# Optimization experiments

Hardware: AMD Instinct MI355X
Metric: run time of the kernel (lower is better)

The kernel has to match this reference:

```python
import jax, jax.numpy as jnp
from jax import lax
import numpy as np

D_MODEL = 512
D_STATE = 16
D_CONV = 4
EXPAND = 2
D_INNER = EXPAND * D_MODEL  # 1024
DT_RANK = (D_MODEL + 15) // 16  # 32
FF_DIM = 1024
N_LAYERS = 2
B, L = 2, 2048


def setup_inputs() -> dict:
    key = jax.random.key(0)
    ks = jax.random.split(key, 16)
    s = 0.02
    x = jax.random.normal(ks[0], (B, L, D_MODEL), jnp.float32)
    in_proj_w = jax.random.normal(ks[1], (N_LAYERS, 2 * D_INNER, D_MODEL), jnp.float32) * s
    conv_w = jax.random.normal(ks[2], (N_LAYERS, D_INNER, D_CONV), jnp.float32) * 0.3
    conv_b = jax.random.normal(ks[3], (N_LAYERS, D_INNER), jnp.float32) * s
    x_proj_w = jax.random.normal(ks[4], (N_LAYERS, DT_RANK + 2 * D_STATE, D_INNER), jnp.float32) * s
    dt_proj_w = jax.random.normal(ks[5], (N_LAYERS, D_INNER, DT_RANK), jnp.float32) * s
    dt_proj_b = jax.random.normal(ks[6], (N_LAYERS, D_INNER), jnp.float32) * 0.5 - 4.0
    A_log = jnp.log(jnp.broadcast_to(jnp.arange(1, D_STATE + 1, dtype=jnp.float32), (N_LAYERS, D_INNER, D_STATE)))
    Dp = jnp.ones((N_LAYERS, D_INNER), jnp.float32)
    out_proj_w = jax.random.normal(ks[7], (N_LAYERS, D_MODEL, D_INNER), jnp.float32) * s
    mlp_w1 = jax.random.normal(ks[8], (FF_DIM, D_MODEL), jnp.float32) * s
    mlp_b1 = jnp.zeros((FF_DIM,), jnp.float32)
    mlp_w2 = jax.random.normal(ks[9], (D_MODEL, FF_DIM), jnp.float32) * s
    mlp_b2 = jnp.zeros((D_MODEL,), jnp.float32)
    return dict(x=x, in_proj_w=in_proj_w, conv_w=conv_w, conv_b=conv_b,
                x_proj_w=x_proj_w, dt_proj_w=dt_proj_w, dt_proj_b=dt_proj_b,
                A_log=A_log, Dp=Dp, out_proj_w=out_proj_w,
                mlp_w1=mlp_w1, mlp_b1=mlp_b1, mlp_w2=mlp_w2, mlp_b2=mlp_b2)


def _mamba_layer(x, ipw, cw, cb, xpw, dpw, dpb, Al, Dv, opw):
    # x: [B, L, d_model]
    b, l, _ = x.shape
    xz = jnp.einsum('bld,ed->ble', x, ipw)           # [B, L, 2*d_inner]
    xin, z = jnp.split(xz, 2, axis=-1)
    # causal depthwise conv1d (pad left d_conv-1)
    xc = jnp.transpose(xin, (0, 2, 1))               # [B, d_inner, L]
    xc = lax.conv_general_dilated(xc, cw[:, None, :], (1,), [(D_CONV - 1, 0)],
                                  feature_group_count=D_INNER)
    xin = jax.nn.silu(jnp.transpose(xc + cb[:, None], (0, 2, 1)))  # [B, L, d_inner]
    dbl = jnp.einsum('bld,ed->ble', xin, xpw)        # [B, L, dt_rank + 2*d_state]
    dt, Bm, Cm = jnp.split(dbl, [DT_RANK, DT_RANK + D_STATE], axis=-1)
    dt = jax.nn.softplus(jnp.einsum('blr,dr->bld', dt, dpw) + dpb)  # [B, L, d_inner]
    A = -jnp.exp(Al)                                  # [d_inner, d_state]
    dA = jnp.exp(dt[..., None] * A)                   # [B, L, d_inner, d_state]
    dBu = dt[..., None] * Bm[:, :, None, :] * xin[..., None]

    def step(h, inp):
        dA_t, dBu_t = inp
        h = dA_t * h + dBu_t
        return h, h

    h0 = jnp.zeros((b, D_INNER, D_STATE), x.dtype)
    _, hs = lax.scan(step, h0, (jnp.moveaxis(dA, 1, 0), jnp.moveaxis(dBu, 1, 0)))
    hs = jnp.moveaxis(hs, 0, 1)                       # [B, L, d_inner, d_state]
    y = jnp.einsum('blds,bls->bld', hs, Cm) + xin * Dv
    y = y * jax.nn.silu(z)
    return jnp.einsum('ble,de->bld', y, opw)


def reference(x, in_proj_w, conv_w, conv_b, x_proj_w, dt_proj_w, dt_proj_b,
              A_log, Dp, out_proj_w, mlp_w1, mlp_b1, mlp_w2, mlp_b2):
    residual = x
    for i in range(N_LAYERS):
        x = _mamba_layer(x, in_proj_w[i], conv_w[i], conv_b[i], x_proj_w[i],
                         dt_proj_w[i], dt_proj_b[i], A_log[i], Dp[i], out_proj_w[i])
    h = x + residual
    h = jax.nn.relu(jnp.einsum('bld,fd->blf', h, mlp_w1) + mlp_b1)  # dropout is identity in eval
    return jnp.einsum('blf,df->bld', h, mlp_w2) + mlp_b2
```

## Files before the change

kernel.cpp:

```cpp
#include <hip/hip_runtime.h>
#include <hip/hip_bf16.h>

#define BB 2
#define LL 2048
#define DMODEL 512
#define DSTATE 16
#define DINNER 1024
#define DTRANK 32
#define FFDIM 1024
#define MTOT (BB*LL)
#define SCL 64
#define NCC 32

typedef unsigned short u16;
typedef __attribute__((ext_vector_type(8))) short bf16x8;
typedef __attribute__((ext_vector_type(4))) float f32x4;

__device__ __forceinline__ float b2f(u16 u){
  unsigned v = ((unsigned)u) << 16; float f; __builtin_memcpy(&f, &v, 4); return f;
}
__device__ __forceinline__ u16 f2b(float f){
  unsigned u; __builtin_memcpy(&u, &f, 4);
  unsigned r = (u + 0x7FFFu + ((u >> 16) & 1u)) >> 16;
  return (u16)r;
}
__device__ __forceinline__ float siluf(float x){ return x / (1.f + __expf(-x)); }
__device__ __forceinline__ float softplusf(float v){
  return fmaxf(v, 0.f) + __logf(1.f + __expf(-fabsf(v)));
}

__device__ __forceinline__ float ldin(const void* p, size_t i, int bf){
  if (bf) return b2f(((const u16*)p)[i]);
  return ((const float*)p)[i];
}
__device__ __forceinline__ void stout(void* p, size_t i, int bf, float v){
  if (bf) ((u16*)p)[i] = f2b(v);
  else    ((float*)p)[i] = v;
}

__device__ __forceinline__ int getbf(const void* dp){
  return (*(const unsigned*)dp == 0x3F803F80u) ? 1 : 0;
}

template<int CVT>
__device__ __forceinline__ bf16x8 ld8(const void* P, size_t gi, int bf){
  if (!CVT || bf) return *(const bf16x8*)((const u16*)P + gi);
  float4 f0 = *(const float4*)((const float*)P + gi);
  float4 f1 = *(const float4*)((const float*)P + gi + 4);
  union { u16 u[8]; bf16x8 v; } t;
  t.u[0]=f2b(f0.x); t.u[1]=f2b(f0.y); t.u[2]=f2b(f0.z); t.u[3]=f2b(f0.w);
  t.u[4]=f2b(f1.x); t.u[5]=f2b(f1.y); t.u[6]=f2b(f1.z); t.u[7]=f2b(f1.w);
  return t.v;
}

#define CVT_IPW (2*2*DINNER*DMODEL)
#define CVT_XPW (2*64*DINNER)
#define CVT_DPW (2*DINNER*DTRANK)
#define CVT_OPW (2*DMODEL*DINNER)
#define CVT_W1  (FFDIM*DMODEL)
#define CVT_W2  (DMODEL*FFDIM)
#define CVT_CW  (2*DINNER*4)
#define CVT_CB  (2*DINNER)
#define CVT_TOT (CVT_IPW+CVT_XPW+CVT_DPW+CVT_OPW+CVT_W1+CVT_W2+CVT_CW+CVT_CB)
__global__ __launch_bounds__(256) void cvt_all_k(
    const void* __restrict__ ipw, const void* __restrict__ xpw,
    const void* __restrict__ dpw, const void* __restrict__ opw,
    const void* __restrict__ w1, const void* __restrict__ w2,
    const void* __restrict__ cw, const void* __restrict__ cb,
    u16* __restrict__ dst, const void* __restrict__ dprobe)
{
  const int bf = getbf(dprobe);
  size_t i4 = ((size_t)blockIdx.x * 256 + threadIdx.x) * 4;
  if (i4 >= CVT_TOT) return;
  const void* src; size_t off = i4;
  if      (off < CVT_IPW)                     { src = ipw; }
  else if ((off -= CVT_IPW) < CVT_XPW)        { src = xpw; }
  else if ((off -= CVT_XPW) < CVT_DPW)        { src = dpw; }
  else if ((off -= CVT_DPW) < CVT_OPW)        { src = opw; }
  else if ((off -= CVT_OPW) < CVT_W1)         { src = w1; }
  else if ((off -= CVT_W1)  < CVT_W2)         { src = w2; }
  else if ((off -= CVT_W2)  < CVT_CW)         { src = cw; }
  else     { off -= CVT_CW;                     src = cb; }
  ushort4 o;
  if (bf) {
    o = *(const ushort4*)((const u16*)src + off);
  } else {
    float4 f = *(const float4*)((const float*)src + off);
    o.x = f2b(f.x); o.y = f2b(f.y); o.z = f2b(f.z); o.w = f2b(f.w);
  }
  *(ushort4*)(dst + i4) = o;
}

template<int ACT, int CVA, int CVW, int CIN, int BM, int BN, int KB, int RESID>
__global__ __launch_bounds__(256) void gemm_mfma(
    const void* __restrict__ A, size_t aoff, int lda,
    const void* __restrict__ W, size_t woff,
    const void* __restrict__ bias, size_t boff,
    void* __restrict__ C, size_t coff, int ldc, int K,
    const void* __restrict__ xres, size_t xroff,
    const void* __restrict__ dprobe)
{
  const int bf = getbf(dprobe);
  constexpr int C8  = KB / 8;
  constexpr int TR  = 256 / C8;
  constexpr int ALD = BM / TR;
  constexpr int WLD = BN / TR;
  __shared__ __align__(16) u16 As[2][BM * KB];
  __shared__ __align__(16) u16 Ws[2][BN * KB];
  const int tid = threadIdx.x;
  const int row0 = blockIdx.y * BM, col0 = blockIdx.x * BN;
  const int wave = tid >> 6, lane = tid & 63;
  const int l15 = lane & 15, quad = lane >> 4;
  constexpr int WMT = (BM == 64) ? 1 : ((BN == 128) ? 4 : 2);
  const int mbase = (BM == 64) ? (wave * 16)
                  : ((BN == 128) ? (wave & 1) * 64 : wave * 32);
  const int nbase = (BM == 128 && BN == 128) ? (wave >> 1) * 64 : 0;

  const int rT = tid / C8, csw = tid % C8;
  const int scg = (KB == 32) ? (csw ^ ((rT >> 1) & 3)) : (csw ^ (rT & 7));
  const int lws = tid * 8;
  const size_t ab0 = aoff + (size_t)(row0 + rT) * lda + scg * 8;
  const size_t wb0 = woff + (size_t)(col0 + rT) * K   + scg * 8;

  f32x4 acc[WMT][4];
#pragma unroll
  for (int i = 0; i < WMT; i++)
#pragma unroll
    for (int j = 0; j < 4; j++) acc[i][j] = (f32x4){0.f,0.f,0.f,0.f};

  const int NT = K / KB;

  auto fchunk = [&](int r_, int g){
    return (KB == 32) ? (g ^ ((r_ >> 1) & 3)) : (g ^ (r_ & 7));
  };
  auto compute = [&](int cur_){
#pragma unroll
    for (int ks = 0; ks < KB / 32; ks++) {
      bf16x8 af_[WMT], bf_[4];
#pragma unroll
      for (int mt = 0; mt < WMT; mt++) {
        int r_ = mbase + mt * 16 + l15;
        af_[mt] = *(const bf16x8*)&As[cur_][r_ * KB + fchunk(r_, ks * 4 + quad) * 8];
      }
#pragma unroll
      for (int nt = 0; nt < 4; nt++) {
        int r_ = nbase + nt * 16 + l15;
        bf_[nt] = *(const bf16x8*)&Ws[cur_][r_ * KB + fchunk(r_, ks * 4 + quad) * 8];
      }
#pragma unroll
      for (int mt = 0; mt < WMT; mt++)
#pragma unroll
        for (int nt = 0; nt < 4; nt++)
          acc[mt][nt] = __builtin_amdgcn_mfma_f32_16x16x32_bf16(af_[mt], bf_[nt], acc[mt][nt], 0, 0, 0);
    }
  };

  bf16x8 ra0[ALD], rw0[WLD], ra1[ALD], rw1[WLD];

#define GLOAD(RA, RW, T) do { const int k1_ = (T) * KB;                        \
  _Pragma("unroll") for (int i = 0; i < ALD; i++)                              \
    RA[i] = ld8<CVA>(A, ab0 + k1_ + (size_t)i * TR * lda, bf);                 \
  _Pragma("unroll") for (int i = 0; i < WLD; i++)                              \
    RW[i] = ld8<CVW>(W, wb0 + k1_ + (size_t)i * TR * K, bf); } while (0)

#define GSTEP(RA, RW, T) do {                                                  \
  const int cur_ = (T) & 1;                                                    \
  _Pragma("unroll") for (int i = 0; i < ALD; i++)                              \
    *(bf16x8*)&As[cur_][lws + i * 2048] = RA[i];                               \
  _Pragma("unroll") for (int i = 0; i < WLD; i++)                              \
    *(bf16x8*)&Ws[cur_][lws + i * 2048] = RW[i];                               \
  if ((T) + 2 < NT) GLOAD(RA, RW, (T) + 2);                                    \
  __syncthreads();                                                             \
  compute(cur_);                                                               \
} while (0)

  GLOAD(ra0, rw0, 0);
  if (NT > 1) GLOAD(ra1, rw1, 1);
  int t = 0;
  for (; t + 1 < NT; t += 2) { GSTEP(ra0, rw0, t); GSTEP(ra1, rw1, t + 1); }
  if (t < NT) GSTEP(ra0, rw0, t);
#undef GLOAD
#undef GSTEP

#pragma unroll
  for (int nt = 0; nt < 4; nt++) {
    int c = col0 + nbase + nt * 16 + l15;
    float bv = bias ? ldin(bias, boff + c, bf) : 0.f;
#pragma unroll
    for (int mt = 0; mt < WMT; mt++) {
      int rb = row0 + mbase + mt * 16 + quad * 4;
#pragma unroll
      for (int r = 0; r < 4; r++) {
        float v = acc[mt][nt][r] + bv;
        if (ACT == 1) v = softplusf(v);
        if (ACT == 2) v = fmaxf(v, 0.f);
        size_t ci = (size_t)(rb + r) * ldc + c;
        if (RESID) v += ldin(xres, xroff + ci, bf);
        if (CIN) stout(C, coff + ci, bf, v);
        else     ((u16*)C)[coff + ci] = f2b(v);
      }
    }
  }
}

template<int FST>
__global__ __launch_bounds__(256) void conv_k(
    const u16* __restrict__ xz, const void* __restrict__ cw, size_t cwo,
    const void* __restrict__ cb, size_t cbo, u16* __restrict__ xc,
    const void* __restrict__ dprobe)
{
  if (FST) {
    const u16* cw16 = (const u16*)cw;
    const u16* cb16 = (const u16*)cb;
    int idx8 = (blockIdx.x * 256 + threadIdx.x) * 8;
    int d8 = idx8 & 1023;
    int row = idx8 >> 10;
    int lb = row & (LL - 1);
    bf16x8 cwv0 = *(const bf16x8*)&cw16[cwo + d8*4];
    bf16x8 cwv1 = *(const bf16x8*)&cw16[cwo + d8*4 + 8];
    bf16x8 cwv2 = *(const bf16x8*)&cw16[cwo + d8*4 + 16];
    bf16x8 cwv3 = *(const bf16x8*)&cw16[cwo + d8*4 + 24];
    bf16x8 cbv  = *(const bf16x8*)&cb16[cbo + d8];
    bf16x8 xv0 = (bf16x8){0,0,0,0,0,0,0,0}, xv1 = xv0, xv2 = xv0, xv3 = xv0;
    if (lb >= 3) xv0 = *(const bf16x8*)&xz[(size_t)(row - 3) * 2048 + d8];
    if (lb >= 2) xv1 = *(const bf16x8*)&xz[(size_t)(row - 2) * 2048 + d8];
    if (lb >= 1) xv2 = *(const bf16x8*)&xz[(size_t)(row - 1) * 2048 + d8];
    xv3 = *(const bf16x8*)&xz[(size_t)row * 2048 + d8];
    bf16x8 ov;
#pragma unroll
    for (int i = 0; i < 8; i++) {
      float acc = b2f((u16)cbv[i]);
      int c0 = i * 4;
      float w0 = b2f((u16)((c0 < 8) ? cwv0[c0 & 7] : (c0 < 16) ? cwv1[c0 & 7] : (c0 < 24) ? cwv2[c0 & 7] : cwv3[c0 & 7]));
      float w1_ = b2f((u16)(((c0+1) < 8) ? cwv0[(c0+1) & 7] : ((c0+1) < 16) ? cwv1[(c0+1) & 7] : ((c0+1) < 24) ? cwv2[(c0+1) & 7] : cwv3[(c0+1) & 7]));
      float w2_ = b2f((u16)(((c0+2) < 8) ? cwv0[(c0+2) & 7] : ((c0+2) < 16) ? cwv1[(c0+2) & 7] : ((c0+2) < 24) ? cwv2[(c0+2) & 7] : cwv3[(c0+2) & 7]));
      float w3_ = b2f((u16)(((c0+3) < 8) ? cwv0[(c0+3) & 7] : ((c0+3) < 16) ? cwv1[(c0+3) & 7] : ((c0+3) < 24) ? cwv2[(c0+3) & 7] : cwv3[(c0+3) & 7]));
      acc += w0 * b2f((u16)xv0[i]);
      acc += w1_ * b2f((u16)xv1[i]);
      acc += w2_ * b2f((u16)xv2[i]);
      acc += w3_ * b2f((u16)xv3[i]);
      ov[i] = (short)f2b(siluf(acc));
    }
    *(bf16x8*)&xc[idx8] = ov;
  } else {
    const int bf = getbf(dprobe);
    int idx = blockIdx.x * 256 + threadIdx.x;
    int d = idx & 1023;
    int row = idx >> 10;
    int lb = row & (LL - 1);
    float acc = ldin(cb, cbo + d, bf);
#pragma unroll
    for (int k = 0; k < 4; k++) {
      int lk = lb - 3 + k;
      if (lk >= 0) acc += ldin(cw, cwo + d*4 + k, bf) * b2f(xz[(size_t)(row - 3 + k) * 2048 + d]);
    }
    xc[idx] = f2b(siluf(acc));
  }
}

template<int CVW>
__global__ __launch_bounds__(256) void scan_A_k(
    const u16* __restrict__ xc,
    const u16* __restrict__ dbl,
    const void* __restrict__ dpwp, size_t dpwo,
    const void* __restrict__ dpbp, size_t dpbo,
    const void* __restrict__ Alog, size_t alo,
    float* __restrict__ Pc, float* __restrict__ Sc,
    const void* __restrict__ dprobe)
{
  const int bf = getbf(dprobe);
  int bid = blockIdx.x;
  int b = bid >> 9;
  int c = (bid >> 4) & (NCC - 1);
  int g = bid & 15;
  int t = threadIdx.x;
  int dl = t >> 2, sq = t & 3;
  int d0 = g * 64, d = d0 + dl;
  int rowb = b * LL + c * SCL;

  __shared__ __align__(16) u16 dts[64 * 64];
  __shared__ __align__(16) u16 us[64 * 64];
  __shared__ __align__(16) float Bs[64 * 20];
  u16* dbls = dts;
  u16* dpws = dts + 64 * 32;

  {
    int r = t >> 2, c8 = (t & 3) * 8;
    *(bf16x8*)&dbls[r * 32 + c8] =
        *(const bf16x8*)&dbl[(size_t)(rowb + r) * 64 + c8];
    *(bf16x8*)&dpws[r * 32 + c8] =
        ld8<CVW>(dpwp, dpwo + (size_t)(d0 + r) * DTRANK + c8, bf);
  }
#pragma unroll
  for (int p = 0; p < 2; p++) {
    int seg = p * 256 + t;
    int r = seg >> 3, c8 = (seg & 7) * 8;
    bf16x8 uv = *(const bf16x8*)&xc[(size_t)(rowb + r) * 1024 + d0 + c8];
    int coff = r >> 3, roff = r & 7;
#pragma unroll
    for (int i = 0; i < 8; i++) {
      int dd = c8 + i;
      us[dd * 64 + ((coff ^ (dd & 7)) << 3) + roff] = (u16)uv[i];
    }
  }
  if (t < 128) {
    int l = t >> 1, grp = t & 1;
    bf16x8 v = *(const bf16x8*)&dbl[(size_t)(rowb + l) * 64 + 32 + grp * 8];
    f32x4 f0 = {b2f((u16)v[0]), b2f((u16)v[1]), b2f((u16)v[2]), b2f((u16)v[3])};
    f32x4 f1 = {b2f((u16)v[4]), b2f((u16)v[5]), b2f((u16)v[6]), b2f((u16)v[7])};
    *(f32x4*)&Bs[l * 20 + grp * 8]     = f0;
    *(f32x4*)&Bs[l * 20 + grp * 8 + 4] = f1;
  }
  float Av[4];
#pragma unroll
  for (int j = 0; j < 4; j++)
    Av[j] = -__expf(ldin(Alog, alo + (size_t)d * DSTATE + sq * 4 + j, bf));
  __syncthreads();

  {
    int wv = t >> 6, lane = t & 63;
    int fl = lane & 15, qd = lane >> 4;
    bf16x8 afr  = *(const bf16x8*)&dbls[(wv * 16 + fl) * 32 + qd * 8];
    bf16x8 bfr0 = *(const bf16x8*)&dpws[(fl)      * 32 + qd * 8];
    bf16x8 bfr1 = *(const bf16x8*)&dpws[(16 + fl) * 32 + qd * 8];
    bf16x8 bfr2 = *(const bf16x8*)&dpws[(32 + fl) * 32 + qd * 8];
    bf16x8 bfr3 = *(const bf16x8*)&dpws[(48 + fl) * 32 + qd * 8];
    __syncthreads();
    f32x4 zz = {0.f, 0.f, 0.f, 0.f};
    f32x4 a0 = __builtin_amdgcn_mfma_f32_16x16x32_bf16(afr, bfr0, zz, 0, 0, 0);
    f32x4 a1 = __builtin_amdgcn_mfma_f32_16x16x32_bf16(afr, bfr1, zz, 0, 0, 0);
    f32x4 a2 = __builtin_amdgcn_mfma_f32_16x16x32_bf16(afr, bfr2, zz, 0, 0, 0);
    f32x4 a3 = __builtin_amdgcn_mfma_f32_16x16x32_bf16(afr, bfr3, zz, 0, 0, 0);
    int lc = wv * 2 + (qd >> 1);
    int off = (qd & 1) * 4;
#define DTWR(AN, NT) do {                                                      \
    int dd_ = (NT) * 16 + fl;                                                  \
    float bvv_ = ldin(dpbp, dpbo + d0 + dd_, bf);                              \
    ushort4 pk_;                                                               \
    pk_.x = f2b(softplusf(AN[0] + bvv_));                                      \
    pk_.y = f2b(softplusf(AN[1] + bvv_));                                      \
    pk_.z = f2b(softplusf(AN[2] + bvv_));                                      \
    pk_.w = f2b(softplusf(AN[3] + bvv_));                                      \
    *(ushort4*)&dts[dd_ * 64 + ((lc ^ (dd_ & 7)) << 3) + off] = pk_; } while (0)
    DTWR(a0, 0); DTWR(a1, 1); DTWR(a2, 2); DTWR(a3, 3);
#undef DTWR
  }
  __syncthreads();

  float h[4] = {0.f,0.f,0.f,0.f}, P[4] = {1.f,1.f,1.f,1.f};
  for (int cc = 0; cc < 8; cc++) {
    int base = dl * 64 + ((cc ^ (dl & 7)) << 3);
    bf16x8 dt8 = *(const bf16x8*)&dts[base];
    bf16x8 u8  = *(const bf16x8*)&us[base];
#pragma unroll
    for (int i = 0; i < 8; i++) {
      int l = cc * 8 + i;
      float dtv = b2f((u16)dt8[i]);
      float uv  = b2f((u16)u8[i]);
      float dtu = dtv * uv;
      f32x4 B4 = *(const f32x4*)&Bs[l * 20 + sq * 4];
#pragma unroll
      for (int j = 0; j < 4; j++) {
        float dA = __expf(dtv * Av[j]);
        h[j] = dA * h[j] + dtu * B4[j];
        P[j] *= dA;
      }
    }
  }
  size_t o = (((size_t)b * DINNER + d) * NCC + c) * DSTATE + sq * 4;
  *(f32x4*)&Pc[o] = (f32x4){P[0], P[1], P[2], P[3]};
  *(f32x4*)&Sc[o] = (f32x4){h[0], h[1], h[2], h[3]};
}

__global__ __launch_bounds__(256) void scan_B_k(
    float* __restrict__ Pc, const float* __restrict__ Sc)
{
  int idx = blockIdx.x * 256 + threadIdx.x;
  int bd = idx >> 4, s = idx & 15;
  float h = 0.f;
  for (int c = 0; c < NCC; c++) {
    size_t o = ((size_t)bd * NCC + c) * DSTATE + s;
    float P = Pc[o], S = Sc[o];
    Pc[o] = h;
    h = P * h + S;
  }
}

template<int CVW>
__global__ __launch_bounds__(256) void scan_C_k(
    u16* __restrict__ dtp, int sdt, const u16* __restrict__ xz,
    const u16* __restrict__ xc,
    const u16* __restrict__ dbl,
    const void* __restrict__ dpwp, size_t dpwo,
    const void* __restrict__ dpbp, size_t dpbo,
    const void* __restrict__ Alog, size_t alo,
    const void* __restrict__ Dpt, size_t dpo, const float* __restrict__ Hinit,
    const void* __restrict__ dprobe)
{
  const int bf = getbf(dprobe);
  int bid = blockIdx.x;
  int b = bid >> 9;
  int c = (bid >> 4) & (NCC - 1);
  int g = bid & 15;
  int t = threadIdx.x;
  int dl = t >> 2, sq = t & 3;
  int d0 = g * 64, d = d0 + dl;
  int rowb = b * LL + c * SCL;

  __shared__ __align__(16) u16 dts[64 * 64];
  __shared__ __align__(16) u16 us[64 * 64];
  __shared__ __align__(16) u16 outs[64 * 64];
  __shared__ __align__(16) float BCs[64 * 36];
  u16* dbls = dts;
  u16* dpws = dts + 64 * 32;

  {
    int r = t >> 2, c8 = (t & 3) * 8;
    *(bf16x8*)&dbls[r * 32 + c8] =
        *(const bf16x8*)&dbl[(size_t)(rowb + r) * 64 + c8];
    *(bf16x8*)&dpws[r * 32 + c8] =
        ld8<CVW>(dpwp, dpwo + (size_t)(d0 + r) * DTRANK + c8, bf);
  }
#pragma unroll
  for (int p = 0; p < 2; p++) {
    int seg = p * 256 + t;
    int r = seg >> 3, c8 = (seg & 7) * 8;
    bf16x8 uv = *(const bf16x8*)&xc[(size_t)(rowb + r) * 1024 + d0 + c8];
    int coff = r >> 3, roff = r & 7;
#pragma unroll
    for (int i = 0; i < 8; i++) {
      int dd = c8 + i;
      us[dd * 64 + ((coff ^ (dd & 7)) << 3) + roff] = (u16)uv[i];
    }
  }
  {
    int l = t >> 2, grp = t & 3;
    bf16x8 v = *(const bf16x8*)&dbl[(size_t)(rowb + l) * 64 + 32 + grp * 8];
    f32x4 f0 = {b2f((u16)v[0]), b2f((u16)v[1]), b2f((u16)v[2]), b2f((u16)v[3])};
    f32x4 f1 = {b2f((u16)v[4]), b2f((u16)v[5]), b2f((u16)v[6]), b2f((u16)v[7])};
    *(f32x4*)&BCs[l * 36 + grp * 8]     = f0;
    *(f32x4*)&BCs[l * 36 + grp * 8 + 4] = f1;
  }
  float Av[4];
#pragma unroll
  for (int j = 0; j < 4; j++)
    Av[j] = -__expf(ldin(Alog, alo + (size_t)d * DSTATE + sq * 4 + j, bf));
  float Dv = ldin(Dpt, dpo + d, bf);
  float h[4];
  size_t o = (((size_t)b * DINNER + d) * NCC + c) * DSTATE + sq * 4;
  f32x4 h4 = *(const f32x4*)&Hinit[o];
  h[0] = h4[0]; h[1] = h4[1]; h[2] = h4[2]; h[3] = h4[3];
  __syncthreads();

  {
    int wv = t >> 6, lane = t & 63;
    int fl = lane & 15, qd = lane >> 4;
    bf16x8 afr  = *(const bf16x8*)&dbls[(wv * 16 + fl) * 32 + qd * 8];
    bf16x8 bfr0 = *(const bf16x8*)&dpws[(fl)      * 32 + qd * 8];
    bf16x8 bfr1 = *(const bf16x8*)&dpws[(16 + fl) * 32 + qd * 8];
    bf16x8 bfr2 = *(const bf16x8*)&dpws[(32 + fl) * 32 + qd * 8];
    bf16x8 bfr3 = *(const bf16x8*)&dpws[(48 + fl) * 32 + qd * 8];
    __syncthreads();
    f32x4 zz = {0.f, 0.f, 0.f, 0.f};
    f32x4 a0 = __builtin_amdgcn_mfma_f32_16x16x32_bf16(afr, bfr0, zz, 0, 0, 0);
    f32x4 a1 = __builtin_amdgcn_mfma_f32_16x16x32_bf16(afr, bfr1, zz, 0, 0, 0);
    f32x4 a2 = __builtin_amdgcn_mfma_f32_16x16x32_bf16(afr, bfr2, zz, 0, 0, 0);
    f32x4 a3 = __builtin_amdgcn_mfma_f32_16x16x32_bf16(afr, bfr3, zz, 0, 0, 0);
    int lc = wv * 2 + (qd >> 1);
    int off = (qd & 1) * 4;
#define DTWR(AN, NT) do {                                                      \
    int dd_ = (NT) * 16 + fl;                                                  \
    float bvv_ = ldin(dpbp, dpbo + d0 + dd_, bf);                              \
    ushort4 pk_;                                                               \
    pk_.x = f2b(softplusf(AN[0] + bvv_));                                      \
    pk_.y = f2b(softplusf(AN[1] + bvv_));                                      \
    pk_.z = f2b(softplusf(AN[2] + bvv_));                                      \
    pk_.w = f2b(softplusf(AN[3] + bvv_));                                      \
    *(ushort4*)&dts[dd_ * 64 + ((lc ^ (dd_ & 7)) << 3) + off] = pk_; } while (0)
    DTWR(a0, 0); DTWR(a1, 1); DTWR(a2, 2); DTWR(a3, 3);
#undef DTWR
  }
  __syncthreads();

  for (int cc = 0; cc < 8; cc++) {
    int base = dl * 64 + ((cc ^ (dl & 7)) << 3);
    bf16x8 dt8 = *(const bf16x8*)&dts[base];
    bf16x8 u8  = *(const bf16x8*)&us[base];
#pragma unroll
    for (int i = 0; i < 8; i++) {
      int l = cc * 8 + i;
      float dtv = b2f((u16)dt8[i]);
      float uv  = b2f((u16)u8[i]);
      float dtu = dtv * uv;
      f32x4 B4 = *(const f32x4*)&BCs[l * 36 + sq * 4];
      f32x4 C4 = *(const f32x4*)&BCs[l * 36 + 16 + sq * 4];
      float y = 0.f;
#pragma unroll
      for (int j = 0; j < 4; j++) {
        float dA = __expf(dtv * Av[j]);
        h[j] = dA * h[j] + dtu * B4[j];
        y += h[j] * C4[j];
      }
      y += __shfl_xor(y, 1);
      y += __shfl_xor(y, 2);
      if (sq == 0) outs[l * 64 + dl] = f2b(y + uv * Dv);
    }
  }
  __syncthreads();
#pragma unroll
  for (int p = 0; p < 2; p++) {
    int seg = p * 256 + t;
    int r = seg >> 3, c8 = (seg & 7) * 8;
    bf16x8 yv = *(const bf16x8*)&outs[r * 64 + c8];
    bf16x8 zv = *(const bf16x8*)&xz[(size_t)(rowb + r) * 2048 + 1024 + d0 + c8];
    bf16x8 ov;
#pragma unroll
    for (int i = 0; i < 8; i++) {
      float z = b2f((u16)zv[i]);
      ov[i] = (short)f2b(b2f((u16)yv[i]) * siluf(z));
    }
    *(bf16x8*)&dtp[(size_t)(rowb + r) * sdt + d0 + c8] = ov;
  }
}

extern "C" void kernel_launch(void* const* d_in, const int* in_sizes, int n_in,
                              void* d_out, int out_size, void* d_ws, size_t ws_size,
                              hipStream_t stream) {
  const void* x_in = d_in[0];
  const void* ipw  = d_in[1];
  const void* cw   = d_in[2];
  const void* cb   = d_in[3];
  const void* xpw  = d_in[4];
  const void* dpw  = d_in[5];
  const void* dpb  = d_in[6];
  const void* Alog = d_in[7];
  const void* Dpt  = d_in[8];
  const void* opw  = d_in[9];
  const void* w1   = d_in[10];
  const void* b1   = d_in[11];
  const void* w2   = d_in[12];
  const void* b2   = d_in[13];

  const bool full = ws_size >= (size_t)64 * 1024 * 1024;
  const bool bfh = (in_sizes[1] == (int)(CVT_IPW * 2));

  if (full) {
    float* Pc = (float*)((char*)d_ws + 64);
    float* Sc = Pc + (size_t)BB*DINNER*NCC*DSTATE;
    u16* p = (u16*)(Sc + (size_t)BB*DINNER*NCC*DSTATE);
    u16* cvt0  = p;
    u16* ipw16 = p;  p += (size_t)CVT_IPW;
    u16* xpw16 = p;  p += (size_t)CVT_XPW;
    u16* dpw16 = p;  p += (size_t)CVT_DPW;
    u16* opw16 = p;  p += (size_t)CVT_OPW;
    u16* w116  = p;  p += (size_t)CVT_W1;
    u16* w216  = p;  p += (size_t)CVT_W2;
    u16* cw16  = p;  p += (size_t)CVT_CW;
    u16* cb16  = p;  p += (size_t)CVT_CB;
    u16* xz    = p;  p += (size_t)MTOT*2*DINNER;
    u16* xc    = p;  p += (size_t)MTOT*DINNER;
    u16* dty   = p;  p += (size_t)MTOT*DINNER;
    u16* dbl   = p;
    u16* bx = xc;
    u16* resid = xz;
    u16* hid = xz + (size_t)4*1024*1024;

    const u16* Wipw = bfh ? (const u16*)ipw : ipw16;
    const u16* Wxpw = bfh ? (const u16*)xpw : xpw16;
    const u16* Wdpw = bfh ? (const u16*)dpw : dpw16;
    const u16* Wopw = bfh ? (const u16*)opw : opw16;
    const u16* Ww1  = bfh ? (const u16*)w1  : w116;
    const u16* Ww2  = bfh ? (const u16*)w2  : w216;
    const u16* Wcw  = bfh ? (const u16*)cw  : cw16;
    const u16* Wcb  = bfh ? (const u16*)cb  : cb16;
    if (!bfh)
      cvt_all_k<<<(CVT_TOT/4 + 255)/256, 256, 0, stream>>>(
          ipw, xpw, dpw, opw, w1, w2, cw, cb, cvt0, Dpt);

    for (int layer = 0; layer < 2; layer++) {
      size_t ipw_o = (size_t)layer*2*DINNER*DMODEL;
      size_t cw_o  = (size_t)layer*DINNER*4,  cb_o = (size_t)layer*DINNER;
      size_t xpw_o = (size_t)layer*64*DINNER, dpw_o = (size_t)layer*DINNER*DTRANK;
      size_t dpb_o = (size_t)layer*DINNER,    al_o = (size_t)layer*DINNER*DSTATE;
      size_t dp_o  = (size_t)layer*DINNER,    opw_o = (size_t)layer*DMODEL*DINNER;
      if (layer == 0)
        gemm_mfma<0,1,0,0,128,64,32,0><<<dim3(32, 32), 256, 0, stream>>>(
            x_in, 0, DMODEL, Wipw, ipw_o, nullptr, 0, xz, 0, 2048, DMODEL,
            nullptr, 0, Dpt);
      else
        gemm_mfma<0,0,0,0,128,64,32,0><<<dim3(32, 32), 256, 0, stream>>>(
            bx, 0, DMODEL, Wipw, ipw_o, nullptr, 0, xz, 0, 2048, DMODEL,
            nullptr, 0, Dpt);
      conv_k<1><<<MTOT*DINNER/2048, 256, 0, stream>>>(
          xz, Wcw, cw_o, Wcb, cb_o, xc, Dpt);
      gemm_mfma<0,0,0,0,64,64,32,0><<<dim3(1, 64), 256, 0, stream>>>(
          xc, 0, DINNER, Wxpw, xpw_o, nullptr, 0, dbl, 0, 64, DINNER,
          nullptr, 0, Dpt);
      scan_A_k<0><<<BB*NCC*16, 256, 0, stream>>>(
          xc, dbl, Wdpw, dpw_o, dpb, dpb_o, Alog, al_o, Pc, Sc, Dpt);
      scan_B_k<<<BB*64, 256, 0, stream>>>(Pc, Sc);
      scan_C_k<0><<<BB*NCC*16, 256, 0, stream>>>(
          dty, 1024, xz, xc, dbl, Wdpw, dpw_o, dpb, dpb_o, Alog, al_o,
          Dpt, dp_o, Pc, Dpt);
      if (layer == 0)
        gemm_mfma<0,0,0,0,64,64,32,0><<<dim3(8, 64), 256, 0, stream>>>(
            dty, 0, 1024, Wopw, opw_o, nullptr, 0, bx, 0, DMODEL, DINNER,
            nullptr, 0, Dpt);
      else
        gemm_mfma<0,0,0,0,64,64,32,1><<<dim3(8, 64), 256, 0, stream>>>(
            dty, 0, 1024, Wopw, opw_o, nullptr, 0, resid, 0, DMODEL, DINNER,
            x_in, 0, Dpt);
    }
    gemm_mfma<2,0,0,0,64,64,32,0><<<dim3(16, 64), 256, 0, stream>>>(
        resid, 0, DMODEL, Ww1, 0, b1, 0, hid, 0, FFDIM, DMODEL,
        nullptr, 0, Dpt);
    gemm_mfma<0,0,0,1,64,64,32,0><<<dim3(8, 64), 256, 0, stream>>>(
        hid, 0, FFDIM, Ww2, 0, b2, 0, d_out, 0, DMODEL, FFDIM,
        nullptr, 0, Dpt);
  } else {
    float* Pc = (float*)((char*)d_ws + 64);
    float* Sc = Pc + (size_t)DINNER*NCC*DSTATE;
    u16* p = (u16*)(Sc + (size_t)DINNER*NCC*DSTATE);
    u16* xz  = p;  p += (size_t)LL*2*DINNER;
    u16* xc  = p;  p += (size_t)LL*DINNER;
    u16* bxF = p;  p += (size_t)MTOT*DMODEL;
    u16* dbl = p;
    u16* hid = xz + (size_t)2*1024*1024;

    for (int layer = 0; layer < 2; layer++) {
      size_t ipw_o = (size_t)layer*2*DINNER*DMODEL;
      size_t cw_o  = (size_t)layer*DINNER*4,  cb_o = (size_t)layer*DINNER;
      size_t xpw_o = (size_t)layer*64*DINNER, dpw_o = (size_t)layer*DINNER*DTRANK;
      size_t dpb_o = (size_t)layer*DINNER,    al_o = (size_t)layer*DINNER*DSTATE;
      size_t dp_o  = (size_t)layer*DINNER,    opw_o = (size_t)layer*DMODEL*DINNER;
      for (int b = 0; b < BB; b++) {
        size_t ro = (size_t)b * LL * DMODEL;
        if (layer == 0)
          gemm_mfma<0,1,1,0,128,128,32,0><<<dim3(16, 16), 256, 0, stream>>>(
              x_in, ro, DMODEL, ipw, ipw_o, nullptr, 0, xz, 0, 2048, DMODEL,
              nullptr, 0, Dpt);
        else
          gemm_mfma<0,0,1,0,128,128,32,0><<<dim3(16, 16), 256, 0, stream>>>(
              bxF, ro, DMODEL, ipw, ipw_o, nullptr, 0, xz, 0, 2048, DMODEL,
              nullptr, 0, Dpt);
        conv_k<0><<<LL*DINNER/256, 256, 0, stream>>>(xz, cw, cw_o, cb, cb_o, xc, Dpt);
        gemm_mfma<0,0,1,0,64,64,32,0><<<dim3(1, 32), 256, 0, stream>>>(
            xc, 0, DINNER, xpw, xpw_o, nullptr, 0, dbl, 0, 64, DINNER,
            nullptr, 0, Dpt);
        scan_A_k<1><<<NCC*16, 256, 0, stream>>>(
            xc, dbl, dpw, dpw_o, dpb, dpb_o, Alog, al_o, Pc, Sc, Dpt);
        scan_B_k<<<64, 256, 0, stream>>>(Pc, Sc);
        scan_C_k<1><<<NCC*16, 256, 0, stream>>>(
            xz, 2048, xz, xc, dbl, dpw, dpw_o, dpb, dpb_o, Alog, al_o,
            Dpt, dp_o, Pc, Dpt);
        if (layer == 0)
          gemm_mfma<0,0,1,0,64,64,32,0><<<dim3(8, 32), 256, 0, stream>>>(
              xz, 0, 2048, opw, opw_o, nullptr, 0, bxF, ro, DMODEL, DINNER,
              nullptr, 0, Dpt);
        else
          gemm_mfma<0,0,1,0,64,64,32,1><<<dim3(8, 32), 256, 0, stream>>>(
              xz, 0, 2048, opw, opw_o, nullptr, 0, bxF, ro, DMODEL, DINNER,
              x_in, ro, Dpt);
      }
    }
    for (int b = 0; b < BB; b++) {
      size_t ro = (size_t)b * LL * DMODEL;
      gemm_mfma<2,0,1,0,64,64,32,0><<<dim3(16, 32), 256, 0, stream>>>(
          bxF, ro, DMODEL, w1, 0, b1, 0, hid, 0, FFDIM, DMODEL,
          nullptr, 0, Dpt);
      gemm_mfma<0,0,1,1,64,64,32,0><<<dim3(8, 32), 256, 0, stream>>>(
          hid, 0, FFDIM, w2, 0, b2, 0, d_out, ro, DMODEL, FFDIM,
          nullptr, 0, Dpt);
    }
  }
}
```

Before: 340.9 us.

## Restructure GEMM main loop with single register stage and widen in_proj tile

The GEMM main loop now uses a single set of staging registers instead of two. Each iteration computes on the current LDS buffer, then writes the next tile into the other LDS buffer and issues global loads two tiles ahead. This lowers register pressure and changes how global loads overlap with MFMA work. Separately, the in_proj GEMM moves from 128x64 to 128x128 tiles, which halves the grid and increases reuse per block at the cost of fewer blocks in flight.

```diff
diff --git a/kernel.cpp b/kernel.cpp
--- a/kernel.cpp
+++ b/kernel.cpp
@@ -155,32 +155,34 @@
     }
   };
 
-  bf16x8 ra0[ALD], rw0[WLD], ra1[ALD], rw1[WLD];
-
-#define GLOAD(RA, RW, T) do { const int k1_ = (T) * KB;                        \
+  bf16x8 ra[ALD], rw[WLD];
+
+#define GLOAD(T) do { const int k1_ = (T) * KB;                                \
   _Pragma("unroll") for (int i = 0; i < ALD; i++)                              \
-    RA[i] = ld8<CVA>(A, ab0 + k1_ + (size_t)i * TR * lda, bf);                 \
+    ra[i] = ld8<CVA>(A, ab0 + k1_ + (size_t)i * TR * lda, bf);                 \
   _Pragma("unroll") for (int i = 0; i < WLD; i++)                              \
-    RW[i] = ld8<CVW>(W, wb0 + k1_ + (size_t)i * TR * K, bf); } while (0)
-
-#define GSTEP(RA, RW, T) do {                                                  \
-  const int cur_ = (T) & 1;                                                    \
+    rw[i] = ld8<CVW>(W, wb0 + k1_ + (size_t)i * TR * K, bf); } while (0)
+
+#define LDSW(BUF) do {                                                         \
   _Pragma("unroll") for (int i = 0; i < ALD; i++)                              \
-    *(bf16x8*)&As[cur_][lws + i * 2048] = RA[i];                               \
+    *(bf16x8*)&As[BUF][lws + i * 2048] = ra[i];                                \
   _Pragma("unroll") for (int i = 0; i < WLD; i++)                              \
-    *(bf16x8*)&Ws[cur_][lws + i * 2048] = RW[i];                               \
-  if ((T) + 2 < NT) GLOAD(RA, RW, (T) + 2);                                    \
-  __syncthreads();                                                             \
-  compute(cur_);                                                               \
-} while (0)
-
-  GLOAD(ra0, rw0, 0);
-  if (NT > 1) GLOAD(ra1, rw1, 1);
-  int t = 0;
-  for (; t + 1 < NT; t += 2) { GSTEP(ra0, rw0, t); GSTEP(ra1, rw1, t + 1); }
-  if (t < NT) GSTEP(ra0, rw0, t);
+    *(bf16x8*)&Ws[BUF][lws + i * 2048] = rw[i]; } while (0)
+
+  GLOAD(0);
+  LDSW(0);
+  __syncthreads();
+  if (NT > 1) GLOAD(1);
+  for (int t = 0; t < NT; ++t) {
+    compute(t & 1);
+    if (t + 1 < NT) {
+      LDSW((t + 1) & 1);
+      __syncthreads();
+      if (t + 2 < NT) GLOAD(t + 2);
+    }
+  }
 #undef GLOAD
-#undef GSTEP
+#undef LDSW
 
 #pragma unroll
   for (int nt = 0; nt < 4; nt++) {
@@ -584,11 +586,11 @@
       size_t dpb_o = (size_t)layer*DINNER,    al_o = (size_t)layer*DINNER*DSTATE;
       size_t dp_o  = (size_t)layer*DINNER,    opw_o = (size_t)layer*DMODEL*DINNER;
       if (layer == 0)
-        gemm_mfma<0,1,0,0,128,64,32,0><<<dim3(32, 32), 256, 0, stream>>>(
+        gemm_mfma<0,1,0,0,128,128,32,0><<<dim3(16, 32), 256, 0, stream>>>(
             x_in, 0, DMODEL, Wipw, ipw_o, nullptr, 0, xz, 0, 2048, DMODEL,
             nullptr, 0, Dpt);
       else
-        gemm_mfma<0,0,0,0,128,64,32,0><<<dim3(32, 32), 256, 0, stream>>>(
+        gemm_mfma<0,0,0,0,128,128,32,0><<<dim3(16, 32), 256, 0, stream>>>(
             bx, 0, DMODEL, Wipw, ipw_o, nullptr, 0, xz, 0, 2048, DMODEL,
             nullptr, 0, Dpt);
       conv_k<1><<<MTOT*DINNER/2048, 256, 0, stream>>>(
```

Result: slower. 351.4 us (+3.1%).
